# Kernel tuning notes

Measured on AMD Instinct MI355X. Metric: run time of the kernel, lower is better.

The kernel has to match this reference:

```python
import jax, jax.numpy as jnp
import numpy as np

ALPHA = 0.2
NEG = -9e15
LAYER_OUT = 2


def gat_layer(h, adj, W, a, concat):
    # h: (b,n,in), W: (in,out), a: (2*out,)
    # Faithful to GATLayer: e[i,j] = leaky_relu(a1.Wh_i + a2.Wh_j), computed
    # without materializing the (b,N,N,2F) repeat_interleave tensor.
    Wh = h @ W                               # (b,n,F)
    F = Wh.shape[-1]
    src = jnp.einsum('bnf,f->bn', Wh, a[:F])  # a1 . Wh_i
    dst = jnp.einsum('bnf,f->bn', Wh, a[F:])  # a2 . Wh_j
    e = jax.nn.leaky_relu(src[:, :, None] + dst[:, None, :], ALPHA)  # (b,n,n)
    att = jax.nn.softmax(jnp.where(adj > 0, e, NEG), axis=-1)
    hp = jnp.einsum('bij,bjf->bif', att, Wh)  # bmm aggregation
    return jax.nn.elu(hp) if concat else hp


def setup_inputs() -> dict:
    key = jax.random.key(0)
    ks = jax.random.split(key, 16)
    b, N, L = 16, 512, 1024
    comp_dim, prot_dim, gat_dim, H, latent = 128, 128, 64, 4, 128
    num_atom, num_amino, layer_cnn, window = 100, 30, 3, 5
    k = 2 * window + 1
    s = 0.1
    inp = {
        'atoms': jax.random.randint(ks[0], (b, N), 0, num_atom),
        'atoms_mask': jnp.ones((b, N), jnp.float32),
        'adjacency': jax.random.randint(ks[1], (b, N, N), 0, 2).astype(jnp.int32),
        'amino': jax.random.randint(ks[2], (b, L), 0, num_amino),
        'amino_mask': jnp.ones((b, L), jnp.float32),
        'E_atom': jax.random.normal(ks[3], (num_atom, comp_dim)) * s,
        'E_amino': jax.random.normal(ks[4], (num_amino, prot_dim)) * s,
        'W_gat': jax.random.normal(ks[5], (H, comp_dim, gat_dim)) * s,
        'a_gat': jax.random.normal(ks[6], (H, 2 * gat_dim)) * s,
        'W_go': jax.random.normal(ks[7], (gat_dim * H, comp_dim)) * s,
        'a_go': jax.random.normal(ks[8], (2 * comp_dim,)) * s,
        'W_comp_w': jax.random.normal(ks[9], (latent, comp_dim)) * s,
        'W_comp_b': jnp.zeros((latent,), jnp.float32),
        'conv_w': jax.random.normal(ks[10], (layer_cnn, 1, 1, k, k)) * s,
        'conv_b': jnp.zeros((layer_cnn, 1), jnp.float32),
        'W_att_w': jax.random.normal(ks[11], (latent, latent)) * s,
        'W_att_b': jnp.zeros((latent,), jnp.float32),
        'pred_w': jax.random.normal(ks[12], (1, 2 * latent)) * s,
        'pred_b': jnp.zeros((1,), jnp.float32),
    }
    return inp


def reference(atoms, atoms_mask, adjacency, amino, amino_mask,
              E_atom, E_amino, W_gat, a_gat, W_go, a_go,
              W_comp_w, W_comp_b, conv_w, conv_b,
              W_att_w, W_att_b, pred_w, pred_b):
    # ---- comp_gat (eval mode: dropout is identity) ----
    av = E_atom[atoms]                                      # (b,N,comp_dim)
    H = W_gat.shape[0]
    heads = [gat_layer(av, adjacency, W_gat[i], a_gat[i], True) for i in range(H)]
    multi = jnp.concatenate(heads, axis=-1)                 # (b,N,H*gat_dim)
    x = jax.nn.elu(gat_layer(multi, adjacency, W_go, a_go, False))
    atoms_vec = jax.nn.leaky_relu(x @ W_comp_w.T + W_comp_b, ALPHA)  # (b,N,latent)
    # ---- prot_cnn ----
    pv = E_amino[amino][:, None, :, :]                      # (b,1,L,prot_dim)
    for i in range(conv_w.shape[0]):
        pv = jax.nn.relu(
            jax.lax.conv_general_dilated(
                pv, conv_w[i], (1, 1), 'SAME',
                dimension_numbers=('NCHW', 'OIHW', 'NCHW'))
            + conv_b[i][None, :, None, None])
    amino_vec = pv[:, 0]                                    # (b,L,prot_dim)
    # ---- bidirectional_attention_prediction ----
    a_v = jax.nn.leaky_relu(atoms_vec @ W_att_w.T + W_att_b, ALPHA)
    p_v = jax.nn.leaky_relu(amino_vec @ W_att_w.T + W_att_b, ALPHA)
    prot = (p_v * amino_mask[:, :, None]).sum(1) / amino_mask.sum(1, keepdims=True)
    comp = (a_v * atoms_mask[:, :, None]).sum(1) / atoms_mask.sum(1, keepdims=True)
    cp = jnp.concatenate([comp, prot], axis=1)              # (b,2*latent)
    for _ in range(LAYER_OUT):
        cp = jax.nn.leaky_relu(cp, ALPHA)
    return cp @ pred_w.T + pred_b                           # (b,1)
```

## Files before the change

kernel.cpp:

```cpp
#include <hip/hip_runtime.h>
#include <hip/hip_bf16.h>

typedef __hip_bfloat16 bf16;

#define ALPHA 0.2f
#define NEGV  -9.0e15f

__device__ __forceinline__ float b2f(bf16 x){ return __bfloat162float(x); }
__device__ __forceinline__ bf16  f2b(float x){ return __float2bfloat16(x); }
__device__ __forceinline__ float lrelu(float x){ return x > 0.f ? x : ALPHA*x; }
__device__ __forceinline__ float eluf(float x){ return x > 0.f ? x : expm1f(x); }

#define P_ATOMS_MASK 0
#define P_AMINO_MASK 8192
#define P_E_ATOM     24576
#define P_E_AMINO    37376
#define P_W_GAT      41216
#define P_A_GAT      73984
#define P_W_GO       74496
#define P_A_GO       107264
#define P_W_COMP_W   107520
#define P_W_COMP_B   123904
#define P_CONV_W     124032
#define P_CONV_B     124395
#define P_W_ATT_W    124398
#define P_W_ATT_B    140782
#define P_PRED_W     140910
#define P_PRED_B     141166
#define P_TOTAL      141167

__global__ __launch_bounds__(256) void k_cvt(const void* src, float* dst, int n)
{
    __shared__ int mode;
    const unsigned short* u = (const unsigned short*)src;
    if (threadIdx.x == 0) {
        int lim = n < 64 ? n : 64;
        bool f32like = false;
        for (int i = 0; i < lim; i += 2) {
            unsigned short h = u[i];
            int e = (h >> 7) & 0xFF;
            bool z = (h & 0x7FFF) == 0;
            if (!(z || (e >= 0x66 && e <= 0x88))) f32like = true;
        }
        if (!f32like && lim > 1 && (u[0] & 0x7FFF) == 0 && (u[1] & 0x7FFF) != 0)
            f32like = true;
        mode = f32like ? 1 : 0;
    }
    __syncthreads();
    int idx = blockIdx.x*256 + threadIdx.x;
    if (idx < n)
        dst[idx] = mode ? ((const float*)src)[idx] : b2f(((const bf16*)src)[idx]);
}

__global__ __launch_bounds__(256) void k_gat1_pre(
    const int* __restrict__ atoms, const float* __restrict__ params,
    bf16* __restrict__ Wh1, float* __restrict__ src1, float* __restrict__ dst1)
{
    int bid = blockIdx.x;
    int b = bid >> 9, n = bid & 511;
    int tid = threadIdx.x;
    __shared__ float av[128];
    if (tid < 128) av[tid] = params[P_E_ATOM + atoms[bid]*128 + tid];
    __syncthreads();
    int h = tid >> 6, f = tid & 63;
    const float* Wp = params + P_W_GAT + h*8192 + f;
    float wh = 0.f;
    #pragma unroll 8
    for (int k = 0; k < 128; ++k) wh += av[k] * Wp[k*64];
    Wh1[(size_t)bid*256 + h*64 + f] = f2b(wh);
    float p1 = wh * params[P_A_GAT + h*128 + f];
    float p2 = wh * params[P_A_GAT + h*128 + 64 + f];
    #pragma unroll
    for (int m = 32; m; m >>= 1) { p1 += __shfl_xor(p1, m, 64); p2 += __shfl_xor(p2, m, 64); }
    if (f == 0) { src1[(b*4+h)*512 + n] = p1; dst1[(b*4+h)*512 + n] = p2; }
}

__global__ __launch_bounds__(256) void k_gat1_att4(
    const int* __restrict__ adj, const bf16* __restrict__ Wh1,
    const float* __restrict__ src1, const float* __restrict__ dst1,
    bf16* __restrict__ multi)
{
    int bid = blockIdx.x;
    int b = bid >> 9, i = bid & 511;
    int tid = threadIdx.x;
    int h = tid >> 6, lane = tid & 63;
    __shared__ float att[4][512];
    const int* adjrow = adj + (size_t)bid*512;
    const float* dstp = dst1 + (b*4+h)*512;
    float s_i = src1[(b*4+h)*512 + i];
    float lm = -3.0e38f;
    #pragma unroll
    for (int jj = 0; jj < 8; ++jj) {
        int j = lane + jj*64;
        float e = lrelu(s_i + dstp[j]);
        e = adjrow[j] > 0 ? e : NEGV;
        att[h][j] = e;
        lm = fmaxf(lm, e);
    }
    #pragma unroll
    for (int m = 32; m; m >>= 1) lm = fmaxf(lm, __shfl_xor(lm, m, 64));
    float ls = 0.f;
    #pragma unroll
    for (int jj = 0; jj < 8; ++jj) {
        int j = lane + jj*64;
        float ex = __expf(att[h][j] - lm);
        att[h][j] = ex;
        ls += ex;
    }
    #pragma unroll
    for (int m = 32; m; m >>= 1) ls += __shfl_xor(ls, m, 64);
    float inv = 1.f / ls;
    const bf16* Whp = Wh1 + (size_t)(b*512)*256 + h*64 + lane;
    float a0=0.f, a1=0.f, a2=0.f, a3=0.f;
    for (int j = 0; j < 512; j += 4) {
        a0 += att[h][j]   * b2f(Whp[(size_t)(j)*256]);
        a1 += att[h][j+1] * b2f(Whp[(size_t)(j+1)*256]);
        a2 += att[h][j+2] * b2f(Whp[(size_t)(j+2)*256]);
        a3 += att[h][j+3] * b2f(Whp[(size_t)(j+3)*256]);
    }
    float hp = (a0+a1+a2+a3) * inv;
    multi[(size_t)bid*256 + h*64 + lane] = f2b(eluf(hp));
}

__global__ __launch_bounds__(128) void k_gat2_pre(
    const bf16* __restrict__ multi, const float* __restrict__ params,
    bf16* __restrict__ Wh2, float* __restrict__ src2, float* __restrict__ dst2)
{
    int bid = blockIdx.x;
    int tid = threadIdx.x;
    __shared__ float row[256];
    __shared__ float sr[2][2];
    row[tid]       = b2f(multi[(size_t)bid*256 + tid]);
    row[tid + 128] = b2f(multi[(size_t)bid*256 + tid + 128]);
    __syncthreads();
    const float* Wp = params + P_W_GO;
    float wh = 0.f;
    #pragma unroll 8
    for (int k = 0; k < 256; ++k) wh += row[k] * Wp[k*128 + tid];
    Wh2[(size_t)bid*128 + tid] = f2b(wh);
    float p1 = wh * params[P_A_GO + tid];
    float p2 = wh * params[P_A_GO + 128 + tid];
    #pragma unroll
    for (int m = 32; m; m >>= 1) { p1 += __shfl_xor(p1, m, 64); p2 += __shfl_xor(p2, m, 64); }
    int wid = tid >> 6;
    if ((tid & 63) == 0) { sr[0][wid] = p1; sr[1][wid] = p2; }
    __syncthreads();
    if (tid == 0) src2[bid] = sr[0][0] + sr[0][1];
    if (tid == 1) dst2[bid] = sr[1][0] + sr[1][1];
}

__global__ __launch_bounds__(256) void k_gat2_att(
    const int* __restrict__ adj, const bf16* __restrict__ Wh2,
    const float* __restrict__ src2, const float* __restrict__ dst2,
    bf16* __restrict__ x)
{
    int bid = blockIdx.x;
    int b = bid >> 9;
    int tid = threadIdx.x;
    __shared__ float att[512];
    __shared__ float red[256];
    float s_i = src2[bid];
    const int* adjrow = adj + (size_t)bid*512;
    const float* dstp = dst2 + b*512;
    float lm = -3.0e38f;
    for (int j = tid; j < 512; j += 256) {
        float e = lrelu(s_i + dstp[j]);
        e = adjrow[j] > 0 ? e : NEGV;
        att[j] = e;
        lm = fmaxf(lm, e);
    }
    #pragma unroll
    for (int m = 32; m; m >>= 1) lm = fmaxf(lm, __shfl_xor(lm, m, 64));
    if ((tid & 63) == 0) red[tid >> 6] = lm;
    __syncthreads();
    float M = fmaxf(fmaxf(red[0], red[1]), fmaxf(red[2], red[3]));
    float ls = 0.f;
    for (int j = tid; j < 512; j += 256) {
        float ex = __expf(att[j] - M);
        att[j] = ex;
        ls += ex;
    }
    #pragma unroll
    for (int m = 32; m; m >>= 1) ls += __shfl_xor(ls, m, 64);
    if ((tid & 63) == 0) red[4 + (tid >> 6)] = ls;
    __syncthreads();
    float inv = 1.f / (red[4] + red[5] + red[6] + red[7]);
    int f = tid & 127, c = tid >> 7;
    const bf16* Whp = Wh2 + (size_t)(b*512)*128 + f;
    int j0 = c * 256;
    float a0=0.f, a1=0.f, a2=0.f, a3=0.f;
    for (int j = 0; j < 256; j += 4) {
        a0 += att[j0+j]   * b2f(Whp[(size_t)(j0+j)*128]);
        a1 += att[j0+j+1] * b2f(Whp[(size_t)(j0+j+1)*128]);
        a2 += att[j0+j+2] * b2f(Whp[(size_t)(j0+j+2)*128]);
        a3 += att[j0+j+3] * b2f(Whp[(size_t)(j0+j+3)*128]);
    }
    float part = (a0+a1) + (a2+a3);
    __syncthreads();
    red[tid] = part;
    __syncthreads();
    if (c == 0) {
        float hp = (red[f] + red[f+128]) * inv;
        x[(size_t)bid*128 + f] = f2b(eluf(hp));
    }
}

#define RM_ROWS 32
__global__ __launch_bounds__(256) void k_rowmat_tile(
    const bf16* __restrict__ in, const float* __restrict__ W,
    const float* __restrict__ bias, bf16* __restrict__ outv)
{
    __shared__ float wlds[128*129];
    __shared__ float rlds[RM_ROWS][128];
    int tid = threadIdx.x;
    size_t row0 = (size_t)blockIdx.x * RM_ROWS;
    for (int idx = tid; idx < 16384; idx += 256)
        wlds[(idx >> 7)*129 + (idx & 127)] = W[idx];
    for (int idx = tid; idx < RM_ROWS*128; idx += 256)
        rlds[idx >> 7][idx & 127] = b2f(in[row0*128 + idx]);
    __syncthreads();
    int l = tid & 127, g = tid >> 7;
    float bl = bias[l];
    #pragma unroll
    for (int rg = 0; rg < 16; rg += 4) {
        int r0 = 2*rg + g;
        float a0=0.f, a1=0.f, a2=0.f, a3=0.f;
        for (int k = 0; k < 128; ++k) {
            float w = wlds[l*129 + k];
            a0 += rlds[r0][k]*w;   a1 += rlds[r0+2][k]*w;
            a2 += rlds[r0+4][k]*w; a3 += rlds[r0+6][k]*w;
        }
        outv[(row0 + r0  )*128 + l] = f2b(lrelu(a0+bl));
        outv[(row0 + r0+2)*128 + l] = f2b(lrelu(a1+bl));
        outv[(row0 + r0+4)*128 + l] = f2b(lrelu(a2+bl));
        outv[(row0 + r0+6)*128 + l] = f2b(lrelu(a3+bl));
    }
}

__global__ __launch_bounds__(256) void k_att_acc_tile(
    const bf16* __restrict__ in, const float* __restrict__ W,
    const float* __restrict__ bias, const float* __restrict__ mask,
    float* __restrict__ acc, int per_b)
{
    __shared__ float wlds[128*129];
    __shared__ float rlds[RM_ROWS][128];
    __shared__ float mlds[RM_ROWS];
    __shared__ float psum[128];
    int tid = threadIdx.x;
    size_t row0 = (size_t)blockIdx.x * RM_ROWS;
    int b = (int)(row0 / per_b);
    for (int idx = tid; idx < 16384; idx += 256)
        wlds[(idx >> 7)*129 + (idx & 127)] = W[idx];
    for (int idx = tid; idx < RM_ROWS*128; idx += 256)
        rlds[idx >> 7][idx & 127] = b2f(in[row0*128 + idx]);
    if (tid < RM_ROWS) mlds[tid] = mask[row0 + tid];
    __syncthreads();
    int l = tid & 127, g = tid >> 7;
    float bl = bias[l];
    float vsum = 0.f;
    #pragma unroll
    for (int rg = 0; rg < 16; rg += 4) {
        int r0 = 2*rg + g;
        float a0=0.f, a1=0.f, a2=0.f, a3=0.f;
        for (int k = 0; k < 128; ++k) {
            float w = wlds[l*129 + k];
            a0 += rlds[r0][k]*w;   a1 += rlds[r0+2][k]*w;
            a2 += rlds[r0+4][k]*w; a3 += rlds[r0+6][k]*w;
        }
        vsum += lrelu(a0+bl)*mlds[r0]   + lrelu(a1+bl)*mlds[r0+2]
              + lrelu(a2+bl)*mlds[r0+4] + lrelu(a3+bl)*mlds[r0+6];
    }
    if (g == 1) psum[l] = vsum;
    __syncthreads();
    if (g == 0) atomicAdd(&acc[b*128 + l], vsum + psum[l]);
}

__global__ __launch_bounds__(128) void k_conv(
    const bf16* __restrict__ in, const int* __restrict__ amino,
    const float* __restrict__ params, bf16* __restrict__ out,
    int layer, int first)
{
    int bid = blockIdx.x;
    int b = bid >> 10, i = bid & 1023;
    int tid = threadIdx.x;
    __shared__ float tile[11][139];
    __shared__ float wts[121];
    __shared__ float bias;
    if (tid < 121) wts[tid] = params[P_CONV_W + layer*121 + tid];
    if (tid == 121) bias = params[P_CONV_B + layer];
    for (int idx = tid; idx < 11*138; idx += 128) {
        int r = idx / 138, cc = idx % 138;
        int ri = i + r - 5, cj = cc - 5;
        float v = 0.f;
        if (ri >= 0 && ri < 1024 && cj >= 0 && cj < 128) {
            v = first ? params[P_E_AMINO + amino[b*1024 + ri]*128 + cj]
                      : b2f(in[((size_t)(b*1024 + ri))*128 + cj]);
        }
        tile[r][cc] = v;
    }
    __syncthreads();
    float a = bias;
    #pragma unroll
    for (int di = 0; di < 11; ++di)
        #pragma unroll
        for (int dj = 0; dj < 11; ++dj)
            a += tile[di][tid + dj] * wts[di*11 + dj];
    out[(size_t)bid*128 + tid] = f2b(fmaxf(a, 0.f));
}

__global__ __launch_bounds__(256) void k_final(
    const float* __restrict__ params, const float* __restrict__ acc,
    float* __restrict__ out)
{
    int b = blockIdx.x, tid = threadIdx.x;
    __shared__ float red[256];
    float s = 0.f;
    for (int t = tid; t < 512; t += 256) s += params[P_ATOMS_MASK + b*512 + t];
    #pragma unroll
    for (int m = 32; m; m >>= 1) s += __shfl_xor(s, m, 64);
    if ((tid & 63) == 0) red[tid >> 6] = s;
    __syncthreads();
    float sum_atoms = red[0]+red[1]+red[2]+red[3];
    __syncthreads();
    s = 0.f;
    for (int t = tid; t < 1024; t += 256) s += params[P_AMINO_MASK + b*1024 + t];
    #pragma unroll
    for (int m = 32; m; m >>= 1) s += __shfl_xor(s, m, 64);
    if ((tid & 63) == 0) red[tid >> 6] = s;
    __syncthreads();
    float sum_amino = red[0]+red[1]+red[2]+red[3];
    __syncthreads();
    float val = (tid < 128) ? acc[b*128 + tid] / sum_atoms
                            : acc[2048 + b*128 + (tid-128)] / sum_amino;
    val = lrelu(lrelu(val));
    val *= params[P_PRED_W + tid];
    #pragma unroll
    for (int m = 32; m; m >>= 1) val += __shfl_xor(val, m, 64);
    if ((tid & 63) == 0) red[tid >> 6] = val;
    __syncthreads();
    if (tid == 0) out[b] = red[0]+red[1]+red[2]+red[3] + params[P_PRED_B];
}

extern "C" void kernel_launch(void* const* d_in, const int* in_sizes, int n_in,
                              void* d_out, int out_size, void* d_ws, size_t ws_size,
                              hipStream_t stream)
{
    const int* atoms     = (const int*)d_in[0];
    const int* adjacency = (const int*)d_in[2];
    const int* amino     = (const int*)d_in[3];
    float* out = (float*)d_out;
    (void)in_sizes; (void)n_in; (void)ws_size;

    char* base = (char*)d_ws;
    float* params = (float*)(base + 0);
    float* src1   = (float*)(base + 565248);
    float* dst1   = (float*)(base + 696320);
    float* src2   = (float*)(base + 827392);
    float* dst2   = (float*)(base + 860160);
    float* acc    = (float*)(base + 892928);
    bf16*  A      = (bf16*)(base + 909568);
    bf16*  B      = (bf16*)(base + 5103872);
    bf16*  C      = (bf16*)(base + 9298176);

    bf16* Wh1 = B;
    bf16* multi = C;
    bf16* Wh2 = B;
    bf16* xbuf = B + 1048576;
    bf16* atoms_vec = C;

    hipMemsetAsync(acc, 0, 4096*sizeof(float), stream);

    k_cvt<<< 32, 256, 0, stream>>>(d_in[1],  params + P_ATOMS_MASK, 8192);
    k_cvt<<< 64, 256, 0, stream>>>(d_in[4],  params + P_AMINO_MASK, 16384);
    k_cvt<<< 50, 256, 0, stream>>>(d_in[5],  params + P_E_ATOM,     12800);
    k_cvt<<< 15, 256, 0, stream>>>(d_in[6],  params + P_E_AMINO,    3840);
    k_cvt<<<128, 256, 0, stream>>>(d_in[7],  params + P_W_GAT,      32768);
    k_cvt<<<  2, 256, 0, stream>>>(d_in[8],  params + P_A_GAT,      512);
    k_cvt<<<128, 256, 0, stream>>>(d_in[9],  params + P_W_GO,       32768);
    k_cvt<<<  1, 256, 0, stream>>>(d_in[10], params + P_A_GO,       256);
    k_cvt<<< 64, 256, 0, stream>>>(d_in[11], params + P_W_COMP_W,   16384);
    k_cvt<<<  1, 256, 0, stream>>>(d_in[12], params + P_W_COMP_B,   128);
    k_cvt<<<  2, 256, 0, stream>>>(d_in[13], params + P_CONV_W,     363);
    k_cvt<<<  1, 256, 0, stream>>>(d_in[14], params + P_CONV_B,     3);
    k_cvt<<< 64, 256, 0, stream>>>(d_in[15], params + P_W_ATT_W,    16384);
    k_cvt<<<  1, 256, 0, stream>>>(d_in[16], params + P_W_ATT_B,    128);
    k_cvt<<<  1, 256, 0, stream>>>(d_in[17], params + P_PRED_W,     256);
    k_cvt<<<  1, 256, 0, stream>>>(d_in[18], params + P_PRED_B,     1);

    k_conv<<<16384, 128, 0, stream>>>(nullptr, amino, params, A, 0, 1);
    k_conv<<<16384, 128, 0, stream>>>(A,       amino, params, B, 1, 0);
    k_conv<<<16384, 128, 0, stream>>>(B,       amino, params, A, 2, 0);

    k_gat1_pre<<<8192, 256, 0, stream>>>(atoms, params, Wh1, src1, dst1);
    k_gat1_att4<<<8192, 256, 0, stream>>>(adjacency, Wh1, src1, dst1, multi);

    k_gat2_pre<<<8192, 128, 0, stream>>>(multi, params, Wh2, src2, dst2);
    k_gat2_att<<<8192, 256, 0, stream>>>(adjacency, Wh2, src2, dst2, xbuf);

    k_rowmat_tile<<<256, 256, 0, stream>>>(xbuf, params + P_W_COMP_W,
                                           params + P_W_COMP_B, atoms_vec);

    k_att_acc_tile<<<256, 256, 0, stream>>>(atoms_vec, params + P_W_ATT_W,
                                            params + P_W_ATT_B, params + P_ATOMS_MASK,
                                            acc, 512);
    k_att_acc_tile<<<512, 256, 0, stream>>>(A, params + P_W_ATT_W,
                                            params + P_W_ATT_B, params + P_AMINO_MASK,
                                            acc + 2048, 1024);

    k_final<<<16, 256, 0, stream>>>(params, acc, out);
}
```

Before: 600.7 us.

## Transpose Wh buffers for vectorized attention aggregation and merge param conversion launches

The pre kernels now write Wh1 and Wh2 in feature-major (transposed) order, so each lane in the attention aggregation reads 8 contiguous bf16 values per vector load instead of strided scalars. The sixteen small conversion launches are also folded into two kernels that find their segment by offset. The transposed writes in the pre kernels become strided scatters, and every thread in the prep kernels re-runs the format detection.

```diff
diff --git a/kernel.cpp b/kernel.cpp
--- a/kernel.cpp
+++ b/kernel.cpp
@@ -2,12 +2,16 @@
 #include <hip/hip_bf16.h>
 
 typedef __hip_bfloat16 bf16;
+typedef __attribute__((ext_vector_type(8))) unsigned short ushort8;
 
 #define ALPHA 0.2f
 #define NEGV  -9.0e15f
 
 __device__ __forceinline__ float b2f(bf16 x){ return __bfloat162float(x); }
 __device__ __forceinline__ bf16  f2b(float x){ return __float2bfloat16(x); }
+__device__ __forceinline__ float u2f(unsigned short u){
+    union { unsigned int i; float f; } x; x.i = ((unsigned)u) << 16; return x.f;
+}
 __device__ __forceinline__ float lrelu(float x){ return x > 0.f ? x : ALPHA*x; }
 __device__ __forceinline__ float eluf(float x){ return x > 0.f ? x : expm1f(x); }
 
@@ -29,32 +33,58 @@
 #define P_PRED_B     141166
 #define P_TOTAL      141167
 
-__global__ __launch_bounds__(256) void k_cvt(const void* src, float* dst, int n)
-{
-    __shared__ int mode;
-    const unsigned short* u = (const unsigned short*)src;
-    if (threadIdx.x == 0) {
-        int lim = n < 64 ? n : 64;
-        bool f32like = false;
-        for (int i = 0; i < lim; i += 2) {
-            unsigned short h = u[i];
-            int e = (h >> 7) & 0xFF;
-            bool z = (h & 0x7FFF) == 0;
-            if (!(z || (e >= 0x66 && e <= 0x88))) f32like = true;
-        }
-        if (!f32like && lim > 1 && (u[0] & 0x7FFF) == 0 && (u[1] & 0x7FFF) != 0)
-            f32like = true;
-        mode = f32like ? 1 : 0;
-    }
-    __syncthreads();
+__device__ __forceinline__ int detect_f32(const unsigned short* u, int n)
+{
+    int lim = n < 64 ? n : 64;
+    bool f32like = false;
+    for (int i = 0; i < lim; i += 2) {
+        unsigned short h = u[i];
+        int e = (h >> 7) & 0xFF;
+        bool z = (h & 0x7FFF) == 0;
+        if (!(z || (e >= 0x66 && e <= 0x88))) f32like = true;
+    }
+    if (!f32like && lim > 1 && (u[0] & 0x7FFF) == 0 && (u[1] & 0x7FFF) != 0)
+        f32like = true;
+    return f32like ? 1 : 0;
+}
+__device__ __forceinline__ float cvt_elem(const void* src, int e, int mode)
+{
+    return mode ? ((const float*)src)[e] : b2f(((const bf16*)src)[e]);
+}
+
+__global__ __launch_bounds__(256) void k_prep_a(
+    const void* p0, const void* p1, const void* p2, const void* p3,
+    const void* p4, const void* p5, const void* p6, const void* p7,
+    float* __restrict__ params)
+{
+    const void* ps[8] = {p0,p1,p2,p3,p4,p5,p6,p7};
+    const int offs[9] = {0,8192,24576,37376,41216,73984,74496,107264,107520};
     int idx = blockIdx.x*256 + threadIdx.x;
-    if (idx < n)
-        dst[idx] = mode ? ((const float*)src)[idx] : b2f(((const bf16*)src)[idx]);
+    if (idx >= 107520) return;
+    int k = 0;
+    while (idx >= offs[k+1]) ++k;
+    int mode = detect_f32((const unsigned short*)ps[k], offs[k+1]-offs[k]);
+    params[idx] = cvt_elem(ps[k], idx - offs[k], mode);
+}
+
+__global__ __launch_bounds__(256) void k_prep_b(
+    const void* p0, const void* p1, const void* p2, const void* p3,
+    const void* p4, const void* p5, const void* p6, const void* p7,
+    float* __restrict__ params)
+{
+    const void* ps[8] = {p0,p1,p2,p3,p4,p5,p6,p7};
+    const int offs[9] = {107520,123904,124032,124395,124398,140782,140910,141166,P_TOTAL};
+    int idx = blockIdx.x*256 + threadIdx.x + 107520;
+    if (idx >= P_TOTAL) return;
+    int k = 0;
+    while (idx >= offs[k+1]) ++k;
+    int mode = detect_f32((const unsigned short*)ps[k], offs[k+1]-offs[k]);
+    params[idx] = cvt_elem(ps[k], idx - offs[k], mode);
 }
 
 __global__ __launch_bounds__(256) void k_gat1_pre(
     const int* __restrict__ atoms, const float* __restrict__ params,
-    bf16* __restrict__ Wh1, float* __restrict__ src1, float* __restrict__ dst1)
+    bf16* __restrict__ Wh1T, float* __restrict__ src1, float* __restrict__ dst1)
 {
     int bid = blockIdx.x;
     int b = bid >> 9, n = bid & 511;
@@ -67,7 +97,7 @@
     float wh = 0.f;
     #pragma unroll 8
     for (int k = 0; k < 128; ++k) wh += av[k] * Wp[k*64];
-    Wh1[(size_t)bid*256 + h*64 + f] = f2b(wh);
+    Wh1T[((size_t)(b*4+h)*64 + f)*512 + n] = f2b(wh);
     float p1 = wh * params[P_A_GAT + h*128 + f];
     float p2 = wh * params[P_A_GAT + h*128 + 64 + f];
     #pragma unroll
@@ -76,7 +106,7 @@
 }
 
 __global__ __launch_bounds__(256) void k_gat1_att4(
-    const int* __restrict__ adj, const bf16* __restrict__ Wh1,
+    const int* __restrict__ adj, const bf16* __restrict__ Wh1T,
     const float* __restrict__ src1, const float* __restrict__ dst1,
     bf16* __restrict__ multi)
 {
@@ -110,23 +140,27 @@
     #pragma unroll
     for (int m = 32; m; m >>= 1) ls += __shfl_xor(ls, m, 64);
     float inv = 1.f / ls;
-    const bf16* Whp = Wh1 + (size_t)(b*512)*256 + h*64 + lane;
+    const ushort8* vp = (const ushort8*)(Wh1T + ((size_t)(b*4+h)*64 + lane)*512);
     float a0=0.f, a1=0.f, a2=0.f, a3=0.f;
-    for (int j = 0; j < 512; j += 4) {
-        a0 += att[h][j]   * b2f(Whp[(size_t)(j)*256]);
-        a1 += att[h][j+1] * b2f(Whp[(size_t)(j+1)*256]);
-        a2 += att[h][j+2] * b2f(Whp[(size_t)(j+2)*256]);
-        a3 += att[h][j+3] * b2f(Whp[(size_t)(j+3)*256]);
-    }
-    float hp = (a0+a1+a2+a3) * inv;
+    #pragma unroll 4
+    for (int jj = 0; jj < 64; ++jj) {
+        ushort8 v = vp[jj];
+        const float* ap = &att[h][jj*8];
+        a0 += ap[0]*u2f(v[0]); a1 += ap[1]*u2f(v[1]);
+        a2 += ap[2]*u2f(v[2]); a3 += ap[3]*u2f(v[3]);
+        a0 += ap[4]*u2f(v[4]); a1 += ap[5]*u2f(v[5]);
+        a2 += ap[6]*u2f(v[6]); a3 += ap[7]*u2f(v[7]);
+    }
+    float hp = ((a0+a1) + (a2+a3)) * inv;
     multi[(size_t)bid*256 + h*64 + lane] = f2b(eluf(hp));
 }
 
 __global__ __launch_bounds__(128) void k_gat2_pre(
     const bf16* __restrict__ multi, const float* __restrict__ params,
-    bf16* __restrict__ Wh2, float* __restrict__ src2, float* __restrict__ dst2)
+    bf16* __restrict__ Wh2T, float* __restrict__ src2, float* __restrict__ dst2)
 {
     int bid = blockIdx.x;
+    int b = bid >> 9, n = bid & 511;
     int tid = threadIdx.x;
     __shared__ float row[256];
     __shared__ float sr[2][2];
@@ -137,7 +171,7 @@
     float wh = 0.f;
     #pragma unroll 8
     for (int k = 0; k < 256; ++k) wh += row[k] * Wp[k*128 + tid];
-    Wh2[(size_t)bid*128 + tid] = f2b(wh);
+    Wh2T[((size_t)b*128 + tid)*512 + n] = f2b(wh);
     float p1 = wh * params[P_A_GO + tid];
     float p2 = wh * params[P_A_GO + 128 + tid];
     #pragma unroll
@@ -150,7 +184,7 @@
 }
 
 __global__ __launch_bounds__(256) void k_gat2_att(
-    const int* __restrict__ adj, const bf16* __restrict__ Wh2,
+    const int* __restrict__ adj, const bf16* __restrict__ Wh2T,
     const float* __restrict__ src2, const float* __restrict__ dst2,
     bf16* __restrict__ x)
 {
@@ -186,14 +220,17 @@
     __syncthreads();
     float inv = 1.f / (red[4] + red[5] + red[6] + red[7]);
     int f = tid & 127, c = tid >> 7;
-    const bf16* Whp = Wh2 + (size_t)(b*512)*128 + f;
-    int j0 = c * 256;
+    const ushort8* vp = (const ushort8*)(Wh2T + ((size_t)b*128 + f)*512 + c*256);
+    const float* ap0 = &att[c*256];
     float a0=0.f, a1=0.f, a2=0.f, a3=0.f;
-    for (int j = 0; j < 256; j += 4) {
-        a0 += att[j0+j]   * b2f(Whp[(size_t)(j0+j)*128]);
-        a1 += att[j0+j+1] * b2f(Whp[(size_t)(j0+j+1)*128]);
-        a2 += att[j0+j+2] * b2f(Whp[(size_t)(j0+j+2)*128]);
-        a3 += att[j0+j+3] * b2f(Whp[(size_t)(j0+j+3)*128]);
+    #pragma unroll 4
+    for (int jj = 0; jj < 32; ++jj) {
+        ushort8 v = vp[jj];
+        const float* ap = ap0 + jj*8;
+        a0 += ap[0]*u2f(v[0]); a1 += ap[1]*u2f(v[1]);
+        a2 += ap[2]*u2f(v[2]); a3 += ap[3]*u2f(v[3]);
+        a0 += ap[4]*u2f(v[4]); a1 += ap[5]*u2f(v[5]);
+        a2 += ap[6]*u2f(v[6]); a3 += ap[7]*u2f(v[7]);
     }
     float part = (a0+a1) + (a2+a3);
     __syncthreads();
@@ -362,40 +399,28 @@
     bf16*  B      = (bf16*)(base + 5103872);
     bf16*  C      = (bf16*)(base + 9298176);
 
-    bf16* Wh1 = B;
+    bf16* Wh1T = B;
     bf16* multi = C;
-    bf16* Wh2 = B;
+    bf16* Wh2T = B;
     bf16* xbuf = B + 1048576;
     bf16* atoms_vec = C;
 
     hipMemsetAsync(acc, 0, 4096*sizeof(float), stream);
 
-    k_cvt<<< 32, 256, 0, stream>>>(d_in[1],  params + P_ATOMS_MASK, 8192);
-    k_cvt<<< 64, 256, 0, stream>>>(d_in[4],  params + P_AMINO_MASK, 16384);
-    k_cvt<<< 50, 256, 0, stream>>>(d_in[5],  params + P_E_ATOM,     12800);
-    k_cvt<<< 15, 256, 0, stream>>>(d_in[6],  params + P_E_AMINO,    3840);
-    k_cvt<<<128, 256, 0, stream>>>(d_in[7],  params + P_W_GAT,      32768);
-    k_cvt<<<  2, 256, 0, stream>>>(d_in[8],  params + P_A_GAT,      512);
-    k_cvt<<<128, 256, 0, stream>>>(d_in[9],  params + P_W_GO,       32768);
-    k_cvt<<<  1, 256, 0, stream>>>(d_in[10], params + P_A_GO,       256);
-    k_cvt<<< 64, 256, 0, stream>>>(d_in[11], params + P_W_COMP_W,   16384);
-    k_cvt<<<  1, 256, 0, stream>>>(d_in[12], params + P_W_COMP_B,   128);
-    k_cvt<<<  2, 256, 0, stream>>>(d_in[13], params + P_CONV_W,     363);
-    k_cvt<<<  1, 256, 0, stream>>>(d_in[14], params + P_CONV_B,     3);
-    k_cvt<<< 64, 256, 0, stream>>>(d_in[15], params + P_W_ATT_W,    16384);
-    k_cvt<<<  1, 256, 0, stream>>>(d_in[16], params + P_W_ATT_B,    128);
-    k_cvt<<<  1, 256, 0, stream>>>(d_in[17], params + P_PRED_W,     256);
-    k_cvt<<<  1, 256, 0, stream>>>(d_in[18], params + P_PRED_B,     1);
+    k_prep_a<<<420, 256, 0, stream>>>(d_in[1], d_in[4], d_in[5], d_in[6],
+                                      d_in[7], d_in[8], d_in[9], d_in[10], params);
+    k_prep_b<<<132, 256, 0, stream>>>(d_in[11], d_in[12], d_in[13], d_in[14],
+                                      d_in[15], d_in[16], d_in[17], d_in[18], params);
 
     k_conv<<<16384, 128, 0, stream>>>(nullptr, amino, params, A, 0, 1);
     k_conv<<<16384, 128, 0, stream>>>(A,       amino, params, B, 1, 0);
     k_conv<<<16384, 128, 0, stream>>>(B,       amino, params, A, 2, 0);
 
-    k_gat1_pre<<<8192, 256, 0, stream>>>(atoms, params, Wh1, src1, dst1);
-    k_gat1_att4<<<8192, 256, 0, stream>>>(adjacency, Wh1, src1, dst1, multi);
-
-    k_gat2_pre<<<8192, 128, 0, stream>>>(multi, params, Wh2, src2, dst2);
-    k_gat2_att<<<8192, 256, 0, stream>>>(adjacency, Wh2, src2, dst2, xbuf);
+    k_gat1_pre<<<8192, 256, 0, stream>>>(atoms, params, Wh1T, src1, dst1);
+    k_gat1_att4<<<8192, 256, 0, stream>>>(adjacency, Wh1T, src1, dst1, multi);
+
+    k_gat2_pre<<<8192, 128, 0, stream>>>(multi, params, Wh2T, src2, dst2);
+    k_gat2_att<<<8192, 256, 0, stream>>>(adjacency, Wh2T, src2, dst2, xbuf);
 
     k_rowmat_tile<<<256, 256, 0, stream>>>(xbuf, params + P_W_COMP_W,
                                            params + P_W_COMP_B, atoms_vec);
```

Result: slower. 1.084 ms (+80.5%).
